# Kernel tuning notes

Measured on AMD Instinct MI355X. Metric: run time of the kernel, lower is better.

## Reference

```python
import jax, jax.numpy as jnp
import numpy as np

DIM = 192
D_STATE = 16
D_CONV = 4
EXPAND = 2
D_INNER = DIM * EXPAND          # 384
DT_RANK = (DIM + 15) // 16      # 12
B_SZ, H_SP, W_SP = 4, 64, 64


def setup_inputs() -> dict:
    key = jax.random.key(0)
    ks = jax.random.split(key, 8)
    f = jax.random.normal
    return {
        "x": f(ks[0], (B_SZ, DIM, H_SP, W_SP), jnp.float32),
        "ln_w": jnp.ones((DIM,), jnp.float32),
        "ln_b": jnp.zeros((DIM,), jnp.float32),
        "in_proj_w": f(ks[1], (2 * D_INNER, DIM), jnp.float32) * 0.02,
        "conv_w": f(ks[2], (D_INNER, D_CONV), jnp.float32) * 0.2,
        "conv_b": jnp.zeros((D_INNER,), jnp.float32),
        "x_proj_w": f(ks[3], (DT_RANK + 2 * D_STATE, D_INNER), jnp.float32) * 0.02,
        "dt_proj_w": f(ks[4], (D_INNER, DT_RANK), jnp.float32) * 0.1,
        "dt_proj_b": f(ks[5], (D_INNER,), jnp.float32) * 0.1,
        "A_log": jnp.log(jnp.broadcast_to(
            jnp.arange(1, D_STATE + 1, dtype=jnp.float32), (D_INNER, D_STATE))),
        "D": jnp.ones((D_INNER,), jnp.float32),
        "out_proj_w": f(ks[6], (DIM, D_INNER), jnp.float32) * 0.02,
    }


def _mamba_block(x, ln_w, ln_b, in_proj_w, conv_w, conv_b, x_proj_w,
                 dt_proj_w, dt_proj_b, A_log, D, out_proj_w):
    B, C, H, W = x.shape
    L = H * W
    # [B,C,H,W] -> [B,L,C]
    xf = x.transpose(0, 2, 3, 1).reshape(B, L, C)

    # LayerNorm
    mu = xf.mean(-1, keepdims=True)
    var = ((xf - mu) ** 2).mean(-1, keepdims=True)
    xn = (xf - mu) * jax.lax.rsqrt(var + 1e-5) * ln_w + ln_b

    # in_proj -> xm (ssm branch), z (gate branch)
    xz = xn @ in_proj_w.T                      # [B,L,2*Di]
    xm, z = jnp.split(xz, 2, axis=-1)

    # causal depthwise conv1d over sequence (pad left d_conv-1)
    xc = xm.transpose(0, 2, 1)                 # [B,Di,L]
    xc = jax.lax.conv_general_dilated(
        xc, conv_w[:, None, :], (1,), [(D_CONV - 1, 0)],
        dimension_numbers=("NCH", "OIH", "NCH"),
        feature_group_count=D_INNER)
    xc = xc + conv_b[None, :, None]
    xm = jax.nn.silu(xc.transpose(0, 2, 1))    # [B,L,Di]

    # x_proj -> dt, B, C (input-dependent SSM params)
    dbc = xm @ x_proj_w.T                      # [B,L,dt_rank+2N]
    dt, Bm, Cm = jnp.split(dbc, [DT_RANK, DT_RANK + D_STATE], axis=-1)
    dt = jax.nn.softplus(dt @ dt_proj_w.T + dt_proj_b)  # [B,L,Di]

    A = -jnp.exp(A_log)                        # [Di,N]

    def step(h, inp):
        xt, dtt, Bt, Ct = inp                  # [B,Di],[B,Di],[B,N],[B,N]
        dA = jnp.exp(dtt[..., None] * A)       # [B,Di,N]
        h = h * dA + (dtt * xt)[..., None] * Bt[:, None, :]
        y = jnp.einsum('bdn,bn->bd', h, Ct)
        return h, y

    h0 = jnp.zeros((B, D_INNER, D_STATE), xm.dtype)
    scan_in = (xm.transpose(1, 0, 2), dt.transpose(1, 0, 2),
               Bm.transpose(1, 0, 2), Cm.transpose(1, 0, 2))
    _, ys = jax.lax.scan(step, h0, scan_in)    # [L,B,Di]

    y = ys.transpose(1, 0, 2) + xm * D         # skip term D*x
    y = y * jax.nn.silu(z)                     # gate
    out = y @ out_proj_w.T                     # [B,L,C]

    out = xf + out                             # residual
    return out.reshape(B, H, W, C).transpose(0, 3, 1, 2)


def reference(x, ln_w, ln_b, in_proj_w, conv_w, conv_b, x_proj_w,
              dt_proj_w, dt_proj_b, A_log, D, out_proj_w):
    return _mamba_block(x, ln_w, ln_b, in_proj_w, conv_w, conv_b, x_proj_w,
                        dt_proj_w, dt_proj_b, A_log, D, out_proj_w)
```

## Files before the change

### kernel.cpp

```cpp
#include <hip/hip_runtime.h>
#include <hip/hip_bf16.h>
#include <cstdint>
#include <cmath>

#define DIMC   192
#define DSTATE 16
#define DCONV  4
#define DINNER 384
#define DTRANK 12
#define BSZ    4
#define HSP    64
#define WSP    64
#define LSEQ   4096
#define NTOK   (BSZ*LSEQ)
#define XPN    (DTRANK + 2*DSTATE)
#define XZW    (2*DINNER)
#define LC4    16
#define NCH4   (LSEQ/LC4)

typedef unsigned short ushortT;
using short8 = __attribute__((ext_vector_type(8))) short;
using f32x4  = __attribute__((ext_vector_type(4))) float;

__device__ __forceinline__ float bflo(unsigned u) { return __uint_as_float(u << 16); }
__device__ __forceinline__ float bfhi(unsigned u) { return __uint_as_float(u & 0xffff0000u); }
__device__ __forceinline__ float bf2f(ushortT u) { return __uint_as_float(((unsigned)u) << 16); }
__device__ __forceinline__ unsigned pkbf(float lo, float hi) {
  __hip_bfloat16 l = __float2bfloat16(lo), h = __float2bfloat16(hi);
  return (unsigned)*(ushortT*)&l | ((unsigned)*(ushortT*)&h << 16);
}
#define UNPK8(arr, base, v4)                                        \
  arr[base + 0] = bflo(v4.x); arr[base + 1] = bfhi(v4.x);           \
  arr[base + 2] = bflo(v4.y); arr[base + 3] = bfhi(v4.y);           \
  arr[base + 4] = bflo(v4.z); arr[base + 5] = bfhi(v4.z);           \
  arr[base + 6] = bflo(v4.w); arr[base + 7] = bfhi(v4.w);

__global__ __launch_bounds__(256) void wcvt_kernel(
    const float* __restrict__ w_in, const float* __restrict__ w_x,
    const float* __restrict__ w_out, __hip_bfloat16* __restrict__ wbf) {
  int gid = blockIdx.x * 256 + threadIdx.x;
  float v;
  if (gid < 147456) {
    v = w_in[gid];
  } else if (gid < 147456 + 18432) {
    int e = gid - 147456;
    int r = e / DINNER, c = e % DINNER;
    v = (r < 44) ? w_x[r * DINNER + c] : 0.f;
  } else {
    v = w_out[gid - 147456 - 18432];
  }
  wbf[gid] = __float2bfloat16(v);
}

__global__ __launch_bounds__(512) void ln_kernel(
    const float* __restrict__ x, const float* __restrict__ ln_w,
    const float* __restrict__ ln_b, __hip_bfloat16* __restrict__ xn) {
  __shared__ float xs[DIMC][WSP + 1];
  __shared__ float mu_s[WSP], rs_s[WSP];
  int bh = blockIdx.x;
  int b = bh >> 6, h = bh & 63;
  int tid = threadIdx.x;
  const float* xb = x + (size_t)b * DIMC * LSEQ + (size_t)h * WSP;
  for (int e = tid; e < DIMC * WSP; e += 512) {
    int c = e >> 6, w = e & 63;
    xs[c][w] = xb[(size_t)c * LSEQ + w];
  }
  __syncthreads();
  {
    int w = tid >> 3, p = tid & 7;
    float s = 0.f, s2 = 0.f;
#pragma unroll
    for (int i = 0; i < 24; ++i) {
      float v = xs[p * 24 + i][w];
      s += v; s2 = fmaf(v, v, s2);
    }
    s  += __shfl_xor(s, 1);  s2 += __shfl_xor(s2, 1);
    s  += __shfl_xor(s, 2);  s2 += __shfl_xor(s2, 2);
    s  += __shfl_xor(s, 4);  s2 += __shfl_xor(s2, 4);
    if (p == 0) {
      float mu = s * (1.f / DIMC);
      float var = s2 * (1.f / DIMC) - mu * mu;
      mu_s[w] = mu;
      rs_s[w] = rsqrtf(var + 1e-5f);
    }
  }
  __syncthreads();
  __hip_bfloat16* xo = xn + (size_t)(b * LSEQ + h * WSP) * DIMC;
  for (int e = tid; e < DIMC * WSP; e += 512) {
    int w = e / DIMC, c = e % DIMC;
    xo[(size_t)w * DIMC + c] =
        __float2bfloat16((xs[c][w] - mu_s[w]) * rs_s[w] * ln_w[c] + ln_b[c]);
  }
}

template<int WM, int WN, int FM, int FN, int EPI>
__global__ __launch_bounds__(256) void gemm_bf16(
    const ushortT* __restrict__ A, const ushortT* __restrict__ B,
    void* __restrict__ Cv, const float* __restrict__ xres,
    int K, int Nreal, int ldc) {
  constexpr int BM = WM * FM * 16, BN = WN * FN * 16;
  __shared__ ushortT As[BM][72];
  __shared__ ushortT Bs[BN][72];
  int bm = blockIdx.x * BM, bn = blockIdx.y * BN;
  int tid = threadIdx.x, lane = tid & 63, w = tid >> 6;
  int wm = w / WN, wn = w % WN;
  int lm = lane & 15, lk = lane >> 4;
  const ushortT* Bb = B;
  size_t zoff = 0;
  if constexpr (EPI == 1) {
    size_t zb = blockIdx.z;
    Bb = B + zb * (size_t)LSEQ * K;
    zoff = zb * (size_t)DIMC * LSEQ;
  }
  f32x4 acc[FM][FN];
#pragma unroll
  for (int mi = 0; mi < FM; ++mi)
#pragma unroll
    for (int ni = 0; ni < FN; ++ni) acc[mi][ni] = (f32x4){0.f, 0.f, 0.f, 0.f};

  for (int k0 = 0; k0 < K; k0 += 64) {
    __syncthreads();
    for (int v = tid; v < BM * 8; v += 256) {
      int row = v >> 3, c8 = v & 7;
      *(uint4*)&As[row][c8 * 8] =
          *(const uint4*)(A + (size_t)(bm + row) * K + k0 + c8 * 8);
    }
    for (int v = tid; v < BN * 8; v += 256) {
      int row = v >> 3, c8 = v & 7;
      *(uint4*)&Bs[row][c8 * 8] =
          *(const uint4*)(Bb + (size_t)(bn + row) * K + k0 + c8 * 8);
    }
    __syncthreads();
#pragma unroll
    for (int ks = 0; ks < 2; ++ks) {
      short8 af[FM], bfr[FN];
#pragma unroll
      for (int mi = 0; mi < FM; ++mi)
        af[mi] = *(const short8*)&As[wm * FM * 16 + mi * 16 + lm][ks * 32 + lk * 8];
#pragma unroll
      for (int ni = 0; ni < FN; ++ni)
        bfr[ni] = *(const short8*)&Bs[wn * FN * 16 + ni * 16 + lm][ks * 32 + lk * 8];
#pragma unroll
      for (int mi = 0; mi < FM; ++mi)
#pragma unroll
        for (int ni = 0; ni < FN; ++ni)
          acc[mi][ni] = __builtin_amdgcn_mfma_f32_16x16x32_bf16(
              af[mi], bfr[ni], acc[mi][ni], 0, 0, 0);
    }
  }
#pragma unroll
  for (int mi = 0; mi < FM; ++mi) {
#pragma unroll
    for (int ni = 0; ni < FN; ++ni) {
      int ncol = bn + wn * FN * 16 + ni * 16 + lm;
#pragma unroll
      for (int r = 0; r < 4; ++r) {
        int m = bm + wm * FM * 16 + mi * 16 + lk * 4 + r;
        if constexpr (EPI == 1) {
          size_t aidx = zoff + (size_t)m * LSEQ + ncol;
          ((float*)Cv)[aidx] = xres[aidx] + acc[mi][ni][r];
        } else if constexpr (EPI == 2) {
          if (ncol < Nreal)
            ((__hip_bfloat16*)Cv)[(size_t)m * ldc + ncol] =
                __float2bfloat16(acc[mi][ni][r]);
        } else {
          if (ncol < Nreal) {
            int nc2 = ncol < 12 ? ncol : ncol + 4;
            ((__hip_bfloat16*)Cv)[(size_t)m * ldc + nc2] =
                __float2bfloat16(acc[mi][ni][r]);
          }
        }
      }
    }
  }
}

__global__ __launch_bounds__(256) void conv_silu_kernel(
    const __hip_bfloat16* __restrict__ xz, const float* __restrict__ conv_w,
    const float* __restrict__ conv_b, __hip_bfloat16* __restrict__ xmh) {
  int gid = blockIdx.x * 256 + threadIdx.x;
  int d = gid % DINNER;
  int tok = gid / DINNER;
  int l = tok & (LSEQ - 1);
  const float4 w = *(const float4*)(conv_w + d * 4);
  float acc = conv_b[d];
  const __hip_bfloat16* base = xz + (size_t)tok * XZW + d;
  if (l >= 3) acc = fmaf(w.x, __bfloat162float(base[-3 * XZW]), acc);
  if (l >= 2) acc = fmaf(w.y, __bfloat162float(base[-2 * XZW]), acc);
  if (l >= 1) acc = fmaf(w.z, __bfloat162float(base[-1 * XZW]), acc);
  acc = fmaf(w.w, __bfloat162float(base[0]), acc);
  float s = acc / (1.f + __expf(-acc));
  xmh[gid] = __float2bfloat16(s);
}

__global__ __launch_bounds__(384) void dt_kernel(
    const ushortT* __restrict__ dbc, const __hip_bfloat16* __restrict__ xmh,
    const float* __restrict__ dtw, const float* __restrict__ dtb,
    unsigned* __restrict__ dxpk) {
  int d = threadIdx.x;
  float w12[12];
  *(float4*)&w12[0] = *(const float4*)(dtw + d * 12);
  *(float4*)&w12[4] = *(const float4*)(dtw + d * 12 + 4);
  *(float4*)&w12[8] = *(const float4*)(dtw + d * 12 + 8);
  float bias = dtb[d];
  int tok0 = blockIdx.x * 16;
  for (int tt = 0; tt < 16; ++tt) {
    int tok = tok0 + tt;
    const ushortT* row = dbc + (size_t)tok * 48;
    float v = bias;
#pragma unroll
    for (int j = 0; j < 12; ++j) v = fmaf(bf2f(row[j]), w12[j], v);
    float dt = v > 15.f ? v : __logf(1.f + __expf(v));
    float xmv = __bfloat162float(xmh[(size_t)tok * DINNER + d]);
    dxpk[(size_t)tok * DINNER + d] = pkbf(dt, xmv);
  }
}

__global__ __launch_bounds__(384) void scan_part1(
    const unsigned* __restrict__ dxpk, const ushortT* __restrict__ dbc,
    const float* __restrict__ A_log, unsigned* __restrict__ hpk) {
  __shared__ ushortT dbc_s[16 * 48];
  int d = threadIdx.x, c = blockIdx.x, b = blockIdx.y;
  size_t rowbase = (size_t)b * LSEQ + (size_t)c * LC4;
  if (d < 96) {
    int row = d / 6, q = d % 6;
    ((uint4*)dbc_s)[d] = ((const uint4*)(dbc + (rowbase + row) * 48))[q];
  }
  float Ac2[16];
#pragma unroll
  for (int q = 0; q < 4; ++q) {
    float4 t4 = *(const float4*)(A_log + d * 16 + q * 4);
    Ac2[q * 4 + 0] = -__expf(t4.x) * 1.44269504f;
    Ac2[q * 4 + 1] = -__expf(t4.y) * 1.44269504f;
    Ac2[q * 4 + 2] = -__expf(t4.z) * 1.44269504f;
    Ac2[q * 4 + 3] = -__expf(t4.w) * 1.44269504f;
  }
  float h[16];
#pragma unroll
  for (int n = 0; n < 16; ++n) h[n] = 0.f;
  float sdt = 0.f;
  const unsigned* pkp = dxpk + rowbase * DINNER + d;
  __syncthreads();
#pragma unroll
  for (int t0 = 0; t0 < 16; t0 += 4) {
    unsigned pk[4];
#pragma unroll
    for (int j = 0; j < 4; ++j) pk[j] = pkp[(t0 + j) * DINNER];
#pragma unroll
    for (int j = 0; j < 4; ++j) {
      int t = t0 + j;
      float dtt = bflo(pk[j]), xmv = bfhi(pk[j]);
      sdt += dtt;
      float dx = dtt * xmv;
      const char* bb = (const char*)dbc_s + t * 96;
      uint4 B0 = *(const uint4*)(bb + 32);
      uint4 B1 = *(const uint4*)(bb + 48);
      float Bv[16];
      UNPK8(Bv, 0, B0)
      UNPK8(Bv, 8, B1)
#pragma unroll
      for (int n = 0; n < 16; ++n) {
        float a = __builtin_amdgcn_exp2f(dtt * Ac2[n]);
        h[n] = fmaf(h[n], a, dx * Bv[n]);
      }
    }
  }
  unsigned up[16];
#pragma unroll
  for (int n = 0; n < 16; ++n)
    up[n] = pkbf(h[n], __builtin_amdgcn_exp2f(Ac2[n] * sdt));
  uint4* hp4 = (uint4*)(hpk + (((size_t)b * NCH4 + c) * DINNER + d) * 16);
#pragma unroll
  for (int q = 0; q < 4; ++q) hp4[q] = *(uint4*)&up[q * 4];
}

__global__ __launch_bounds__(256) void scan_part2(
    const unsigned* __restrict__ hpk, ushortT* __restrict__ hinb) {
  int e = blockIdx.x * 256 + threadIdx.x;
  int b = blockIdx.y;
  float H = 0.f;
  size_t base = (size_t)b * NCH4 * (DINNER * DSTATE) + e;
#pragma unroll 16
  for (int c = 0; c < NCH4; ++c) {
    size_t idx = base + (size_t)c * (DINNER * DSTATE);
    unsigned w = hpk[idx];
    __hip_bfloat16 hb = __float2bfloat16(H);
    hinb[idx] = *(ushortT*)&hb;
    H = fmaf(bfhi(w), H, bflo(w));
  }
}

__global__ __launch_bounds__(384) void scan_part3(
    const unsigned* __restrict__ dxpk, const ushortT* __restrict__ dbc,
    const __hip_bfloat16* __restrict__ xz, const float* __restrict__ A_log,
    const float* __restrict__ Dvec, const ushortT* __restrict__ hinb,
    __hip_bfloat16* __restrict__ ybuf) {
  __shared__ ushortT dbc_s[16 * 48];
  int d = threadIdx.x, c = blockIdx.x, b = blockIdx.y;
  size_t rowbase = (size_t)b * LSEQ + (size_t)c * LC4;
  if (d < 96) {
    int row = d / 6, q = d % 6;
    ((uint4*)dbc_s)[d] = ((const uint4*)(dbc + (rowbase + row) * 48))[q];
  }
  float Ac2[16];
#pragma unroll
  for (int q = 0; q < 4; ++q) {
    float4 t4 = *(const float4*)(A_log + d * 16 + q * 4);
    Ac2[q * 4 + 0] = -__expf(t4.x) * 1.44269504f;
    Ac2[q * 4 + 1] = -__expf(t4.y) * 1.44269504f;
    Ac2[q * 4 + 2] = -__expf(t4.z) * 1.44269504f;
    Ac2[q * 4 + 3] = -__expf(t4.w) * 1.44269504f;
  }
  float h[16];
  {
    const uint4* hp = (const uint4*)(hinb + (((size_t)b * NCH4 + c) * DINNER + d) * 16);
    uint4 h0 = hp[0], h1 = hp[1];
    UNPK8(h, 0, h0)
    UNPK8(h, 8, h1)
  }
  float Dd = Dvec[d];
  const unsigned* pkp = dxpk + rowbase * DINNER + d;
  const ushortT* zp = (const ushortT*)xz + rowbase * XZW + DINNER + d;
  __hip_bfloat16* yp = ybuf + rowbase * DINNER + d;
  __syncthreads();
#pragma unroll
  for (int t0 = 0; t0 < 16; t0 += 4) {
    unsigned pk[4];
    ushortT zv4[4];
#pragma unroll
    for (int j = 0; j < 4; ++j) {
      pk[j] = pkp[(t0 + j) * DINNER];
      zv4[j] = zp[(t0 + j) * XZW];
    }
#pragma unroll
    for (int j = 0; j < 4; ++j) {
      int t = t0 + j;
      float dtt = bflo(pk[j]), xmv = bfhi(pk[j]);
      float dx = dtt * xmv;
      const char* bb = (const char*)dbc_s + t * 96;
      uint4 B0 = *(const uint4*)(bb + 32);
      uint4 B1 = *(const uint4*)(bb + 48);
      uint4 C0 = *(const uint4*)(bb + 64);
      uint4 C1 = *(const uint4*)(bb + 80);
      float Bv[16], Cw[16];
      UNPK8(Bv, 0, B0)
      UNPK8(Bv, 8, B1)
      UNPK8(Cw, 0, C0)
      UNPK8(Cw, 8, C1)
      float y0 = 0.f, y1 = 0.f, y2 = 0.f, y3 = 0.f;
#pragma unroll
      for (int n = 0; n < 16; n += 4) {
        float a0 = __builtin_amdgcn_exp2f(dtt * Ac2[n + 0]);
        float a1 = __builtin_amdgcn_exp2f(dtt * Ac2[n + 1]);
        float a2 = __builtin_amdgcn_exp2f(dtt * Ac2[n + 2]);
        float a3 = __builtin_amdgcn_exp2f(dtt * Ac2[n + 3]);
        h[n + 0] = fmaf(h[n + 0], a0, dx * Bv[n + 0]);
        h[n + 1] = fmaf(h[n + 1], a1, dx * Bv[n + 1]);
        h[n + 2] = fmaf(h[n + 2], a2, dx * Bv[n + 2]);
        h[n + 3] = fmaf(h[n + 3], a3, dx * Bv[n + 3]);
        y0 = fmaf(h[n + 0], Cw[n + 0], y0);
        y1 = fmaf(h[n + 1], Cw[n + 1], y1);
        y2 = fmaf(h[n + 2], Cw[n + 2], y2);
        y3 = fmaf(h[n + 3], Cw[n + 3], y3);
      }
      float yv = fmaf(xmv, Dd, (y0 + y1) + (y2 + y3));
      float zv = bf2f(zv4[j]);
      float gt = zv * __builtin_amdgcn_rcpf(
          1.f + __builtin_amdgcn_exp2f(zv * -1.44269504f));
      yp[(size_t)t * DINNER] = __float2bfloat16(yv * gt);
    }
  }
}

extern "C" void kernel_launch(void* const* d_in, const int* in_sizes, int n_in,
                              void* d_out, int out_size, void* d_ws, size_t ws_size,
                              hipStream_t stream) {
  const float* x        = (const float*)d_in[0];
  const float* ln_w     = (const float*)d_in[1];
  const float* ln_b     = (const float*)d_in[2];
  const float* in_proj  = (const float*)d_in[3];
  const float* conv_w   = (const float*)d_in[4];
  const float* conv_b   = (const float*)d_in[5];
  const float* x_proj   = (const float*)d_in[6];
  const float* dt_w     = (const float*)d_in[7];
  const float* dt_b     = (const float*)d_in[8];
  const float* A_log    = (const float*)d_in[9];
  const float* Dvec     = (const float*)d_in[10];
  const float* out_proj = (const float*)d_in[11];
  float* out = (float*)d_out;

  float* ws = (float*)d_ws;
  __hip_bfloat16* xzb  = (__hip_bfloat16*)ws;
  __hip_bfloat16* xmh  = (__hip_bfloat16*)(ws + 6291456);
  ushortT*        dbcb = (ushortT*)(ws + 9437184);
  unsigned*       dxpk = (unsigned*)(ws + 9830400);
  unsigned*       hpk  = (unsigned*)(ws + 16121856);
  ushortT*        hinb = (ushortT*)(ws + 22413312);
  __hip_bfloat16* ybuf = (__hip_bfloat16*)(ws + 25559040);
  __hip_bfloat16* xnbf = (__hip_bfloat16*)(ws + 28704768);
  __hip_bfloat16* wbf  = (__hip_bfloat16*)(ws + 30277632);

  const ushortT* win  = (const ushortT*)wbf;
  const ushortT* wx   = (const ushortT*)(wbf + 147456);
  const ushortT* wout = (const ushortT*)(wbf + 165888);

  wcvt_kernel<<<936, 256, 0, stream>>>(in_proj, x_proj, out_proj, wbf);

  ln_kernel<<<BSZ * HSP, 512, 0, stream>>>(x, ln_w, ln_b, xnbf);

  gemm_bf16<2, 2, 4, 2, 2><<<dim3(NTOK / 128, XZW / 64), 256, 0, stream>>>(
      (const ushortT*)xnbf, win, xzb, nullptr, DIMC, XZW, XZW);

  conv_silu_kernel<<<(NTOK * DINNER) / 256, 256, 0, stream>>>(
      xzb, conv_w, conv_b, xmh);

  gemm_bf16<4, 1, 1, 3, 3><<<dim3(NTOK / 64, 1), 256, 0, stream>>>(
      (const ushortT*)xmh, wx, dbcb, nullptr, DINNER, XPN, 48);

  dt_kernel<<<NTOK / 16, 384, 0, stream>>>(dbcb, xmh, dt_w, dt_b, dxpk);

  scan_part1<<<dim3(NCH4, BSZ), 384, 0, stream>>>(dxpk, dbcb, A_log, hpk);
  scan_part2<<<dim3(DINNER * DSTATE / 256, BSZ), 256, 0, stream>>>(hpk, hinb);
  scan_part3<<<dim3(NCH4, BSZ), 384, 0, stream>>>(
      dxpk, dbcb, xzb, A_log, Dvec, hinb, ybuf);

  gemm_bf16<2, 2, 2, 4, 1><<<dim3(DIMC / 64, LSEQ / 128, BSZ), 256, 0, stream>>>(
      wout, (const ushortT*)ybuf, out, x, DINNER, LSEQ, LSEQ);
}
```

Before: 177.1 us.

## Fold dt_proj into x_proj weights and fuse softplus into GEMM epilogue

Precomputes a combined bf16 weight (dt_proj_w @ x_proj_w rows plus the B/C rows) so a single GEMM yields dt pre-activations and B/C directly. The epilogue applies bias and softplus and packs dt with xm into dxpk, which removes the separate dt_kernel and its reread of dbc and xm. The conv+SiLU kernel is also vectorised to handle 8 channels per thread, and the in_proj GEMM tile is widened. The cost is a GEMM with N=448 instead of 48, and dt now comes from a bf16-rounded product weight, which may shift numerics slightly.

After: 174.7 us. No clear change (-1.3%).

```diff
diff --git a/kernel.cpp b/kernel.cpp
--- a/kernel.cpp
+++ b/kernel.cpp
@@ -17,6 +17,7 @@
 #define XZW    (2*DINNER)
 #define LC4    16
 #define NCH4   (LSEQ/LC4)
+#define NXP    448
 
 typedef unsigned short ushortT;
 using short8 = __attribute__((ext_vector_type(8))) short;
@@ -36,20 +37,26 @@
   arr[base + 6] = bflo(v4.w); arr[base + 7] = bfhi(v4.w);
 
 __global__ __launch_bounds__(256) void wcvt_kernel(
-    const float* __restrict__ w_in, const float* __restrict__ w_x,
-    const float* __restrict__ w_out, __hip_bfloat16* __restrict__ wbf) {
+    const float* __restrict__ w_in, const float* __restrict__ w_out,
+    __hip_bfloat16* __restrict__ wbf) {
   int gid = blockIdx.x * 256 + threadIdx.x;
-  float v;
-  if (gid < 147456) {
-    v = w_in[gid];
-  } else if (gid < 147456 + 18432) {
-    int e = gid - 147456;
-    int r = e / DINNER, c = e % DINNER;
-    v = (r < 44) ? w_x[r * DINNER + c] : 0.f;
-  } else {
-    v = w_out[gid - 147456 - 18432];
-  }
+  float v = gid < 147456 ? w_in[gid] : w_out[gid - 147456];
   wbf[gid] = __float2bfloat16(v);
+}
+
+__global__ __launch_bounds__(256) void wcomb_kernel(
+    const float* __restrict__ xpw, const float* __restrict__ dtw,
+    __hip_bfloat16* __restrict__ wcb) {
+  int gid = blockIdx.x * 256 + threadIdx.x;
+  int dd = gid / 384, k = gid % 384;
+  float v = 0.f;
+  if (dd < 384) {
+#pragma unroll
+    for (int j = 0; j < 12; ++j) v = fmaf(dtw[dd * 12 + j], xpw[j * 384 + k], v);
+  } else if (dd < 416) {
+    v = xpw[(dd - 372) * 384 + k];
+  }
+  wcb[gid] = __float2bfloat16(v);
 }
 
 __global__ __launch_bounds__(512) void ln_kernel(
@@ -96,8 +103,9 @@
 template<int WM, int WN, int FM, int FN, int EPI>
 __global__ __launch_bounds__(256) void gemm_bf16(
     const ushortT* __restrict__ A, const ushortT* __restrict__ B,
-    void* __restrict__ Cv, const float* __restrict__ xres,
-    int K, int Nreal, int ldc) {
+    void* __restrict__ Cv, void* __restrict__ Cv2,
+    const ushortT* __restrict__ xm_aux, const float* __restrict__ bias384,
+    const float* __restrict__ xres, int K, int Nreal, int ldc) {
   constexpr int BM = WM * FM * 16, BN = WN * FN * 16;
   __shared__ ushortT As[BM][72];
   __shared__ ushortT Bs[BN][72];
@@ -164,10 +172,14 @@
             ((__hip_bfloat16*)Cv)[(size_t)m * ldc + ncol] =
                 __float2bfloat16(acc[mi][ni][r]);
         } else {
-          if (ncol < Nreal) {
-            int nc2 = ncol < 12 ? ncol : ncol + 4;
-            ((__hip_bfloat16*)Cv)[(size_t)m * ldc + nc2] =
-                __float2bfloat16(acc[mi][ni][r]);
+          if (ncol < 384) {
+            float dtr = acc[mi][ni][r] + bias384[ncol];
+            float dt = dtr > 15.f ? dtr : __logf(1.f + __expf(dtr));
+            float xmv = bf2f(xm_aux[(size_t)m * DINNER + ncol]);
+            ((unsigned*)Cv)[(size_t)m * DINNER + ncol] = pkbf(dt, xmv);
+          } else if (ncol < 416) {
+            __hip_bfloat16 bv = __float2bfloat16(acc[mi][ni][r]);
+            ((ushortT*)Cv2)[(size_t)m * 48 + 16 + (ncol - 384)] = *(ushortT*)&bv;
           }
         }
       }
@@ -178,42 +190,33 @@
 __global__ __launch_bounds__(256) void conv_silu_kernel(
     const __hip_bfloat16* __restrict__ xz, const float* __restrict__ conv_w,
     const float* __restrict__ conv_b, __hip_bfloat16* __restrict__ xmh) {
-  int gid = blockIdx.x * 256 + threadIdx.x;
-  int d = gid % DINNER;
-  int tok = gid / DINNER;
+  int g8 = blockIdx.x * 256 + threadIdx.x;
+  int d8 = g8 % 48;
+  int tok = g8 / 48;
   int l = tok & (LSEQ - 1);
-  const float4 w = *(const float4*)(conv_w + d * 4);
-  float acc = conv_b[d];
-  const __hip_bfloat16* base = xz + (size_t)tok * XZW + d;
-  if (l >= 3) acc = fmaf(w.x, __bfloat162float(base[-3 * XZW]), acc);
-  if (l >= 2) acc = fmaf(w.y, __bfloat162float(base[-2 * XZW]), acc);
-  if (l >= 1) acc = fmaf(w.z, __bfloat162float(base[-1 * XZW]), acc);
-  acc = fmaf(w.w, __bfloat162float(base[0]), acc);
-  float s = acc / (1.f + __expf(-acc));
-  xmh[gid] = __float2bfloat16(s);
-}
-
-__global__ __launch_bounds__(384) void dt_kernel(
-    const ushortT* __restrict__ dbc, const __hip_bfloat16* __restrict__ xmh,
-    const float* __restrict__ dtw, const float* __restrict__ dtb,
-    unsigned* __restrict__ dxpk) {
-  int d = threadIdx.x;
-  float w12[12];
-  *(float4*)&w12[0] = *(const float4*)(dtw + d * 12);
-  *(float4*)&w12[4] = *(const float4*)(dtw + d * 12 + 4);
-  *(float4*)&w12[8] = *(const float4*)(dtw + d * 12 + 8);
-  float bias = dtb[d];
-  int tok0 = blockIdx.x * 16;
-  for (int tt = 0; tt < 16; ++tt) {
-    int tok = tok0 + tt;
-    const ushortT* row = dbc + (size_t)tok * 48;
-    float v = bias;
-#pragma unroll
-    for (int j = 0; j < 12; ++j) v = fmaf(bf2f(row[j]), w12[j], v);
-    float dt = v > 15.f ? v : __logf(1.f + __expf(v));
-    float xmv = __bfloat162float(xmh[(size_t)tok * DINNER + d]);
-    dxpk[(size_t)tok * DINNER + d] = pkbf(dt, xmv);
-  }
+  int d0 = d8 * 8;
+  const ushortT* base = (const ushortT*)xz + (size_t)tok * XZW + d0;
+  uint4 r0, r1, r2, r3;
+  r3 = *(const uint4*)(base);
+  r2 = l >= 1 ? *(const uint4*)(base - XZW)     : (uint4){0, 0, 0, 0};
+  r1 = l >= 2 ? *(const uint4*)(base - 2 * XZW) : (uint4){0, 0, 0, 0};
+  r0 = l >= 3 ? *(const uint4*)(base - 3 * XZW) : (uint4){0, 0, 0, 0};
+  float x0[8], x1[8], x2[8], x3[8];
+  UNPK8(x0, 0, r0) UNPK8(x1, 0, r1) UNPK8(x2, 0, r2) UNPK8(x3, 0, r3)
+  ushortT outv[8];
+#pragma unroll
+  for (int j = 0; j < 8; ++j) {
+    const float4 w = *(const float4*)(conv_w + (d0 + j) * 4);
+    float acc = conv_b[d0 + j];
+    acc = fmaf(w.x, x0[j], acc);
+    acc = fmaf(w.y, x1[j], acc);
+    acc = fmaf(w.z, x2[j], acc);
+    acc = fmaf(w.w, x3[j], acc);
+    float s = acc / (1.f + __expf(-acc));
+    __hip_bfloat16 sb = __float2bfloat16(s);
+    outv[j] = *(ushortT*)&sb;
+  }
+  *(uint4*)((ushortT*)xmh + (size_t)tok * DINNER + d0) = *(uint4*)outv;
 }
 
 __global__ __launch_bounds__(384) void scan_part1(
@@ -399,25 +402,26 @@
   __hip_bfloat16* ybuf = (__hip_bfloat16*)(ws + 25559040);
   __hip_bfloat16* xnbf = (__hip_bfloat16*)(ws + 28704768);
   __hip_bfloat16* wbf  = (__hip_bfloat16*)(ws + 30277632);
+  __hip_bfloat16* wcb  = (__hip_bfloat16*)(ws + 30388224);
 
   const ushortT* win  = (const ushortT*)wbf;
-  const ushortT* wx   = (const ushortT*)(wbf + 147456);
-  const ushortT* wout = (const ushortT*)(wbf + 165888);
-
-  wcvt_kernel<<<936, 256, 0, stream>>>(in_proj, x_proj, out_proj, wbf);
+  const ushortT* wout = (const ushortT*)(wbf + 147456);
+
+  wcvt_kernel<<<864, 256, 0, stream>>>(in_proj, out_proj, wbf);
+  wcomb_kernel<<<672, 256, 0, stream>>>(x_proj, dt_w, wcb);
 
   ln_kernel<<<BSZ * HSP, 512, 0, stream>>>(x, ln_w, ln_b, xnbf);
 
-  gemm_bf16<2, 2, 4, 2, 2><<<dim3(NTOK / 128, XZW / 64), 256, 0, stream>>>(
-      (const ushortT*)xnbf, win, xzb, nullptr, DIMC, XZW, XZW);
-
-  conv_silu_kernel<<<(NTOK * DINNER) / 256, 256, 0, stream>>>(
+  gemm_bf16<2, 2, 4, 4, 2><<<dim3(NTOK / 128, XZW / 128), 256, 0, stream>>>(
+      (const ushortT*)xnbf, win, xzb, nullptr, nullptr, nullptr, nullptr,
+      DIMC, XZW, XZW);
+
+  conv_silu_kernel<<<(NTOK * DINNER / 8) / 256, 256, 0, stream>>>(
       xzb, conv_w, conv_b, xmh);
 
-  gemm_bf16<4, 1, 1, 3, 3><<<dim3(NTOK / 64, 1), 256, 0, stream>>>(
-      (const ushortT*)xmh, wx, dbcb, nullptr, DINNER, XPN, 48);
-
-  dt_kernel<<<NTOK / 16, 384, 0, stream>>>(dbcb, xmh, dt_w, dt_b, dxpk);
+  gemm_bf16<2, 2, 4, 2, 4><<<dim3(NTOK / 128, NXP / 64), 256, 0, stream>>>(
+      (const ushortT*)xmh, (const ushortT*)wcb, dxpk, dbcb,
+      (const ushortT*)xmh, dt_b, nullptr, DINNER, NXP, 0);
 
   scan_part1<<<dim3(NCH4, BSZ), 384, 0, stream>>>(dxpk, dbcb, A_log, hpk);
   scan_part2<<<dim3(DINNER * DSTATE / 256, BSZ), 256, 0, stream>>>(hpk, hinb);
@@ -425,5 +429,6 @@
       dxpk, dbcb, xzb, A_log, Dvec, hinb, ybuf);
 
   gemm_bf16<2, 2, 2, 4, 1><<<dim3(DIMC / 64, LSEQ / 128, BSZ), 256, 0, stream>>>(
-      wout, (const ushortT*)ybuf, out, x, DINNER, LSEQ, LSEQ);
-}
+      wout, (const ushortT*)ybuf, out, nullptr, nullptr, nullptr, x,
+      DINNER, LSEQ, LSEQ);
+}
```
